# Kernel optimization log

Hardware: AMD Instinct MI355X
Metric: run time of the kernel (lower is better)

Reference implementation:

```python
import jax, jax.numpy as jnp
import numpy as np
from jax import lax

B, IN, H1, H2, NC = 16384, 128, 256, 128, 10
BETA = 0.5
THR = 1.0
SLOPE = 25.0  # snntorch surrogate.fast_sigmoid default slope


@jax.custom_vjp
def spike(x):
    # Heaviside fire with fast-sigmoid surrogate gradient
    return (x > 0).astype(x.dtype)

def _spike_fwd(x):
    return spike(x), x

def _spike_bwd(x, g):
    return (g / (SLOPE * jnp.abs(x) + 1.0) ** 2,)

spike.defvjp(_spike_fwd, _spike_bwd)


def setup_inputs() -> dict:
    key = jax.random.key(0)
    ks = jax.random.split(key, 7)
    def lin(kw, kb, fan_in, fan_out):
        lim = 1.0 / np.sqrt(fan_in)
        W = jax.random.uniform(kw, (fan_out, fan_in), jnp.float32, -lim, lim)
        b = jax.random.uniform(kb, (fan_out,), jnp.float32, -lim, lim)
        return W, b
    W1, b1 = lin(ks[0], ks[1], IN, H1)
    W2, b2 = lin(ks[2], ks[3], H1, H2)
    Wo, bo = lin(ks[4], ks[5], H2, NC)
    x = jax.random.normal(ks[6], (B, IN), jnp.float32)
    return {"x": x, "W1": W1, "b1": b1, "W2": W2, "b2": b2,
            "Wo": Wo, "bo": bo, "num_steps": 20}


def reference(x, W1, b1, W2, b2, Wo, bo, num_steps):
    # fc1(x) is time-invariant -> hoist out of the recurrent loop (same math)
    cur1 = x @ W1.T + b1  # [B, H1]

    def lif(mem, cur):
        # snntorch Leaky (reset_mechanism='subtract'):
        # reset from previous mem (detached), then decay+input, then fire
        reset = lax.stop_gradient((mem > THR).astype(mem.dtype))
        mem = BETA * mem + cur - reset * THR
        spk = spike(mem - THR)
        return spk, mem

    def step(carry, _):
        m1, m2, mo = carry
        s1, m1 = lif(m1, cur1)
        s2, m2 = lif(m2, s1 @ W2.T + b2)
        so, mo = lif(mo, s2 @ Wo.T + bo)
        return (m1, m2, mo), so

    init = (jnp.zeros((B, H1), x.dtype),
            jnp.zeros((B, H2), x.dtype),
            jnp.zeros((B, NC), x.dtype))
    _, spk_rec = lax.scan(step, init, None, length=num_steps)
    return spk_rec.sum(axis=0)  # [B, NC] spike counts
```

## Files before the change

kernel.cpp:

```cpp
#include <hip/hip_runtime.h>
#include <stdint.h>

#define B_TOT 16384
#define IN_DIM 128
#define H1 256
#define H2 128
#define NC 10

#define W2T_BYTES (H1 * H2 * 4)
#define WOT_OFF   W2T_BYTES
#define WOT_BYTES (H2 * NC * 4)
#define SCR_OFF   (WOT_OFF + WOT_BYTES)
#define LDS_BYTES (SCR_OFF + 16 * 1024)

typedef float v2f __attribute__((ext_vector_type(2)));

__global__ __launch_bounds__(256) void gemm1_kernel(
    const float* __restrict__ x, const float* __restrict__ W1,
    const float* __restrict__ b1, float* __restrict__ cur1) {
  __shared__ float xs[16 * 128];
  const int tid = threadIdx.x;
  const long row0 = (long)blockIdx.x * 16;

  const float4* xt = (const float4*)(x + row0 * IN_DIM);
  float4* xs4 = (float4*)xs;
  xs4[tid] = xt[tid];
  xs4[tid + 256] = xt[tid + 256];
  __syncthreads();

  const int n = tid;
  float acc[16];
#pragma unroll
  for (int r = 0; r < 16; ++r) acc[r] = 0.f;

  const float* wrow = W1 + n * IN_DIM;
  for (int k0 = 0; k0 < IN_DIM; k0 += 4) {
    const float4 wv = *(const float4*)(wrow + k0);
#pragma unroll
    for (int r = 0; r < 16; ++r) {
      const float4 xv = *(const float4*)(xs + r * IN_DIM + k0);
      acc[r] = fmaf(wv.x, xv.x, acc[r]);
      acc[r] = fmaf(wv.y, xv.y, acc[r]);
      acc[r] = fmaf(wv.z, xv.z, acc[r]);
      acc[r] = fmaf(wv.w, xv.w, acc[r]);
    }
  }
  const float bias = b1[n];
#pragma unroll
  for (int r = 0; r < 16; ++r)
    cur1[(row0 + r) * H1 + n] = acc[r] + bias;
}

__global__ __launch_bounds__(1024) void transpose_kernel(
    const float* __restrict__ W2, const float* __restrict__ Wo,
    float* __restrict__ W2T, float* __restrict__ WoT) {
  const int idx = blockIdx.x * 1024 + threadIdx.x;
  if (idx < H2 * H1) {
    const int o = idx >> 8;
    const int j = idx & 255;
    W2T[j * H2 + o] = W2[idx];
  } else {
    const int k = idx - H2 * H1;
    if (k < NC * H2) {
      const int o = k >> 7;
      const int j = k & 127;
      WoT[j * NC + o] = Wo[k];
    }
  }
}

__device__ __forceinline__ int mbcnt64(unsigned long long m) {
  return (int)__builtin_amdgcn_mbcnt_hi(
      (unsigned)(m >> 32), __builtin_amdgcn_mbcnt_lo((unsigned)m, 0u));
}

__device__ __noinline__ v2f serial_row(unsigned long long m0,
                                       unsigned long long m1,
                                       unsigned long long m2,
                                       unsigned long long m3,
                                       const char* w2b) {
  v2f acc = {0.f, 0.f};
  while (m0) { const int j = (int)__builtin_ctzll(m0); m0 &= m0 - 1;
    acc += *(const v2f*)(w2b + (j << 9)); }
  while (m1) { const int j = (int)__builtin_ctzll(m1); m1 &= m1 - 1;
    acc += *(const v2f*)(w2b + ((64 + j) << 9)); }
  while (m2) { const int j = (int)__builtin_ctzll(m2); m2 &= m2 - 1;
    acc += *(const v2f*)(w2b + ((128 + j) << 9)); }
  while (m3) { const int j = (int)__builtin_ctzll(m3); m3 &= m3 - 1;
    acc += *(const v2f*)(w2b + ((192 + j) << 9)); }
  return acc;
}

__global__ __launch_bounds__(1024) void snn_kernel(
    const float* __restrict__ cur1, const float* __restrict__ W2Tg,
    const float* __restrict__ WoTg, const float* __restrict__ b2,
    const float* __restrict__ bo, const int* __restrict__ nsp,
    float* __restrict__ out) {
  extern __shared__ float lds[];

  const int tid = threadIdx.x;
  {
    float4* dst = (float4*)lds;
    const float4* src = (const float4*)W2Tg;
#pragma unroll
    for (int i = 0; i < 8; ++i) dst[tid + i * 1024] = src[tid + i * 1024];
    if (tid < 320)
      ((float4*)((char*)lds + WOT_OFF))[tid] = ((const float4*)WoTg)[tid];
  }
  __syncthreads();

  const int w = tid >> 6;
  const int l = tid & 63;
  const int lo = (l < NC) ? l : 0;
  const float bb0 = b2[2 * l];
  const float bb1 = b2[2 * l + 1];
  const float bol = bo[lo];
  const int nsteps = *nsp;

  int* scrA = (int*)((char*)lds + SCR_OFF) + w * 256;
  int* scrB = scrA + 128;
  const char* w2b = (const char*)lds + 8 * l;
  const char* wob = (const char*)lds + WOT_OFF + 4 * lo;

  const int wr0 = l << 9;
  const int wr1 = (64 + l) << 9;
  const int wr2 = (128 + l) << 9;
  const int wr3 = (192 + l) << 9;
  const int or0 = 80 * l;
  const int or1 = 80 * l + 40;

#define LOAD8(P, scrp, kk)                                  \
  const int4 P##ia = *(const int4*)((scrp) + (kk));         \
  const int4 P##ib = *(const int4*)((scrp) + (kk) + 4);     \
  const v2f P##p0 = *(const v2f*)(w2b + P##ia.x);           \
  const v2f P##p1 = *(const v2f*)(w2b + P##ia.y);           \
  const v2f P##p2 = *(const v2f*)(w2b + P##ia.z);           \
  const v2f P##p3 = *(const v2f*)(w2b + P##ia.w);           \
  const v2f P##p4 = *(const v2f*)(w2b + P##ib.x);           \
  const v2f P##p5 = *(const v2f*)(w2b + P##ib.y);           \
  const v2f P##p6 = *(const v2f*)(w2b + P##ib.z);           \
  const v2f P##p7 = *(const v2f*)(w2b + P##ib.w);

#define ADD8(P, acc)                                        \
  acc += P##p0; acc += P##p1; acc += P##p2; acc += P##p3;   \
  acc += P##p4; acc += P##p5; acc += P##p6; acc += P##p7;

#define TAILS(scrp, S, acc)                                 \
  {                                                         \
    int k = ((S) >> 3) << 3;                                \
    if ((S) & 4) {                                          \
      const int4 ia = *(const int4*)((scrp) + k);           \
      const v2f p0 = *(const v2f*)(w2b + ia.x);             \
      const v2f p1 = *(const v2f*)(w2b + ia.y);             \
      const v2f p2 = *(const v2f*)(w2b + ia.z);             \
      const v2f p3 = *(const v2f*)(w2b + ia.w);             \
      acc += p0; acc += p1; acc += p2; acc += p3;           \
      k += 4;                                               \
    }                                                       \
    if ((S) & 2) {                                          \
      const int2 ia = *(const int2*)((scrp) + k);           \
      const v2f p0 = *(const v2f*)(w2b + ia.x);             \
      const v2f p1 = *(const v2f*)(w2b + ia.y);             \
      acc += p0; acc += p1;                                 \
      k += 2;                                               \
    }                                                       \
    if ((S) & 1) {                                          \
      const v2f p0 = *(const v2f*)(w2b + (scrp)[k]);        \
      acc += p0;                                            \
    }                                                       \
  }

#define OLOAD8(P, scrp, kk)                                 \
  const int4 P##ia = *(const int4*)((scrp) + (kk));         \
  const int4 P##ib = *(const int4*)((scrp) + (kk) + 4);     \
  const float P##q0 = *(const float*)(wob + P##ia.x);       \
  const float P##q1 = *(const float*)(wob + P##ia.y);       \
  const float P##q2 = *(const float*)(wob + P##ia.z);       \
  const float P##q3 = *(const float*)(wob + P##ia.w);       \
  const float P##q4 = *(const float*)(wob + P##ib.x);       \
  const float P##q5 = *(const float*)(wob + P##ib.y);       \
  const float P##q6 = *(const float*)(wob + P##ib.z);       \
  const float P##q7 = *(const float*)(wob + P##ib.w);

#define OADD8(P, co)                                        \
  co += P##q0; co += P##q1; co += P##q2; co += P##q3;       \
  co += P##q4; co += P##q5; co += P##q6; co += P##q7;

#define OTAILS(scrp, S, co)                                 \
  {                                                         \
    int k = ((S) >> 3) << 3;                                \
    if ((S) & 4) {                                          \
      const int4 ia = *(const int4*)((scrp) + k);           \
      const float u0 = *(const float*)(wob + ia.x);         \
      const float u1 = *(const float*)(wob + ia.y);         \
      const float u2 = *(const float*)(wob + ia.z);         \
      const float u3 = *(const float*)(wob + ia.w);         \
      co += u0; co += u1; co += u2; co += u3;               \
      k += 4;                                               \
    }                                                       \
    if ((S) & 2) {                                          \
      const int2 ia = *(const int2*)((scrp) + k);           \
      const float u0 = *(const float*)(wob + ia.x);         \
      const float u1 = *(const float*)(wob + ia.y);         \
      co += u0; co += u1;                                   \
      k += 2;                                               \
    }                                                       \
    if ((S) & 1) {                                          \
      co += *(const float*)(wob + (scrp)[k]);               \
    }                                                       \
  }

  for (int rp = 0; rp < 2; ++rp) {
    const long bA = (long)blockIdx.x * 64 + w * 4 + rp * 2;
    const long bB = bA + 1;

    float cA[4], cB[4];
#pragma unroll
    for (int i = 0; i < 4; ++i) {
      cA[i] = cur1[bA * H1 + i * 64 + l];
      cB[i] = cur1[bB * H1 + i * 64 + l];
    }

    float mA1[4] = {0.f, 0.f, 0.f, 0.f}, spA1[4] = {0.f, 0.f, 0.f, 0.f};
    float mB1[4] = {0.f, 0.f, 0.f, 0.f}, spB1[4] = {0.f, 0.f, 0.f, 0.f};
    float mA2a = 0.f, mA2b = 0.f, spA2a = 0.f, spA2b = 0.f;
    float mB2a = 0.f, mB2b = 0.f, spB2a = 0.f, spB2b = 0.f;
    float moA = 0.f, spoA = 0.f, cntA = 0.f;
    float moB = 0.f, spoB = 0.f, cntB = 0.f;

    for (int t = 0; t < nsteps; ++t) {
      unsigned long long gA[4], gB[4];
      bool sA[4], sB[4];
#pragma unroll
      for (int i = 0; i < 4; ++i) {
        mA1[i] = fmaf(0.5f, mA1[i], cA[i]) - spA1[i];
        sA[i] = mA1[i] > 1.0f;
        spA1[i] = sA[i] ? 1.0f : 0.0f;
        gA[i] = __ballot(sA[i]);
        mB1[i] = fmaf(0.5f, mB1[i], cB[i]) - spB1[i];
        sB[i] = mB1[i] > 1.0f;
        spB1[i] = sB[i] ? 1.0f : 0.0f;
        gB[i] = __ballot(sB[i]);
      }
      const int pA0 = (int)__popcll(gA[0]);
      const int pA01 = pA0 + (int)__popcll(gA[1]);
      const int pA012 = pA01 + (int)__popcll(gA[2]);
      const int SA = pA012 + (int)__popcll(gA[3]);
      const int pB0 = (int)__popcll(gB[0]);
      const int pB01 = pB0 + (int)__popcll(gB[1]);
      const int pB012 = pB01 + (int)__popcll(gB[2]);
      const int SB = pB012 + (int)__popcll(gB[3]);

      if (sA[0]) scrA[mbcnt64(gA[0])] = wr0;
      if (sA[1]) scrA[pA0 + mbcnt64(gA[1])] = wr1;
      if (sA[2]) { const int rk = pA01 + mbcnt64(gA[2]);
                   if (rk < 128) scrA[rk] = wr2; }
      if (sA[3]) { const int rk = pA012 + mbcnt64(gA[3]);
                   if (rk < 128) scrA[rk] = wr3; }
      if (sB[0]) scrB[mbcnt64(gB[0])] = wr0;
      if (sB[1]) scrB[pB0 + mbcnt64(gB[1])] = wr1;
      if (sB[2]) { const int rk = pB01 + mbcnt64(gB[2]);
                   if (rk < 128) scrB[rk] = wr2; }
      if (sB[3]) { const int rk = pB012 + mbcnt64(gB[3]);
                   if (rk < 128) scrB[rk] = wr3; }
      asm volatile("s_waitcnt lgkmcnt(0)" ::: "memory");

      v2f accA = {0.f, 0.f}, accB = {0.f, 0.f};
      if (__builtin_expect(SA > 128 || SB > 128, 0)) {
        accA = serial_row(gA[0], gA[1], gA[2], gA[3], w2b);
        accB = serial_row(gB[0], gB[1], gB[2], gB[3], w2b);
      } else {
        const int nA8 = SA >> 3;
        const int nB8 = SB >> 3;
        int ka = 0, kb = 0;
        while (ka < nA8 && kb < nB8) {
          { LOAD8(a_, scrA, ka * 8) LOAD8(b_, scrB, kb * 8)
            ADD8(a_, accA) ADD8(b_, accB) }
          ++ka; ++kb;
        }
        while (ka < nA8) {
          { LOAD8(c_, scrA, ka * 8) ADD8(c_, accA) }
          ++ka;
        }
        while (kb < nB8) {
          { LOAD8(d_, scrB, kb * 8) ADD8(d_, accB) }
          ++kb;
        }
        TAILS(scrA, SA, accA)
        TAILS(scrB, SB, accB)
      }
      const float aA0 = accA.x + bb0;
      const float aA1 = accA.y + bb1;
      const float aB0 = accB.x + bb0;
      const float aB1 = accB.y + bb1;

      mA2a = fmaf(0.5f, mA2a, aA0) - spA2a;
      mA2b = fmaf(0.5f, mA2b, aA1) - spA2b;
      mB2a = fmaf(0.5f, mB2a, aB0) - spB2a;
      mB2b = fmaf(0.5f, mB2b, aB1) - spB2b;
      const bool saA = mA2a > 1.0f, sbA = mA2b > 1.0f;
      const bool saB = mB2a > 1.0f, sbB = mB2b > 1.0f;
      const unsigned long long mAe = __ballot(saA);
      const unsigned long long mAo = __ballot(sbA);
      const unsigned long long mBe = __ballot(saB);
      const unsigned long long mBo = __ballot(sbB);
      spA2a = saA ? 1.0f : 0.0f;
      spA2b = sbA ? 1.0f : 0.0f;
      spB2a = saB ? 1.0f : 0.0f;
      spB2b = sbB ? 1.0f : 0.0f;
      const int pAe = (int)__popcll(mAe);
      const int SoA = pAe + (int)__popcll(mAo);
      const int pBe = (int)__popcll(mBe);
      const int SoB = pBe + (int)__popcll(mBo);

      if (saA) scrA[mbcnt64(mAe)] = or0;
      if (sbA) scrA[pAe + mbcnt64(mAo)] = or1;
      if (saB) scrB[mbcnt64(mBe)] = or0;
      if (sbB) scrB[pBe + mbcnt64(mBo)] = or1;
      asm volatile("s_waitcnt lgkmcnt(0)" ::: "memory");

      float coA = 0.f, coB = 0.f;
      {
        const int nA8 = SoA >> 3;
        const int nB8 = SoB >> 3;
        int ka = 0, kb = 0;
        while (ka < nA8 && kb < nB8) {
          { OLOAD8(e_, scrA, ka * 8) OLOAD8(f_, scrB, kb * 8)
            OADD8(e_, coA) OADD8(f_, coB) }
          ++ka; ++kb;
        }
        while (ka < nA8) {
          { OLOAD8(g_, scrA, ka * 8) OADD8(g_, coA) }
          ++ka;
        }
        while (kb < nB8) {
          { OLOAD8(h_, scrB, kb * 8) OADD8(h_, coB) }
          ++kb;
        }
        OTAILS(scrA, SoA, coA)
        OTAILS(scrB, SoB, coB)
      }
      coA += bol;
      coB += bol;

      moA = fmaf(0.5f, moA, coA) - spoA;
      moB = fmaf(0.5f, moB, coB) - spoB;
      const bool soA = moA > 1.0f;
      const bool soB = moB > 1.0f;
      spoA = soA ? 1.0f : 0.0f;
      spoB = soB ? 1.0f : 0.0f;
      cntA += spoA;
      cntB += spoB;
    }

    if (l < NC) {
      out[bA * NC + l] = cntA;
      out[bB * NC + l] = cntB;
    }
  }
#undef LOAD8
#undef ADD8
#undef TAILS
#undef OLOAD8
#undef OADD8
#undef OTAILS
}

extern "C" void kernel_launch(void* const* d_in, const int* in_sizes, int n_in,
                              void* d_out, int out_size, void* d_ws,
                              size_t ws_size, hipStream_t stream) {
  const float* x  = (const float*)d_in[0];
  const float* W1 = (const float*)d_in[1];
  const float* b1 = (const float*)d_in[2];
  const float* W2 = (const float*)d_in[3];
  const float* b2 = (const float*)d_in[4];
  const float* Wo = (const float*)d_in[5];
  const float* bo = (const float*)d_in[6];
  const int* nsp  = (const int*)d_in[7];
  float* outp = (float*)d_out;

  float* cur1 = (float*)d_ws;
  float* W2Tg = cur1 + (size_t)B_TOT * H1;
  float* WoTg = W2Tg + H1 * H2;

  gemm1_kernel<<<B_TOT / 16, 256, 0, stream>>>(x, W1, b1, cur1);
  transpose_kernel<<<(H2 * H1 + NC * H2 + 1023) / 1024, 1024, 0, stream>>>(
      W2, Wo, W2Tg, WoTg);

  hipFuncSetAttribute((const void*)snn_kernel,
                      hipFuncAttributeMaxDynamicSharedMemorySize, LDS_BYTES);
  snn_kernel<<<256, 1024, LDS_BYTES, stream>>>(cur1, W2Tg, WoTg, b2, bo, nsp,
                                               outp);
}
```

Before: 115.4 us.

## Fuse transpose into gemm1, register-tile gemm1, interleave four rows per wave

Folds the weight transpose into an extra block of the first GEMM launch, which removes one kernel launch. The GEMM now uses 64-row blocks with a 4x16 register tile per thread, so each x load from LDS feeds more FMAs. The SNN kernel processes four batch rows per wave at once instead of two pairs in sequence, giving more independent LDS gathers to overlap latency. The scratch list per row shrinks to 64 entries, with a serial fallback when more than 64 spikes fire; this costs more registers and the fallback path is taken more often.

Measured after the change: 157.0 us. +36.0%, slower.

```diff
diff --git a/kernel.cpp b/kernel.cpp
--- a/kernel.cpp
+++ b/kernel.cpp
@@ -15,57 +15,81 @@
 
 typedef float v2f __attribute__((ext_vector_type(2)));
 
-__global__ __launch_bounds__(256) void gemm1_kernel(
+__global__ __launch_bounds__(256) void gemm1_fused_kernel(
     const float* __restrict__ x, const float* __restrict__ W1,
-    const float* __restrict__ b1, float* __restrict__ cur1) {
-  __shared__ float xs[16 * 128];
+    const float* __restrict__ b1, const float* __restrict__ W2,
+    const float* __restrict__ Wo, float* __restrict__ cur1,
+    float* __restrict__ W2T, float* __restrict__ WoT) {
   const int tid = threadIdx.x;
-  const long row0 = (long)blockIdx.x * 16;
-
+  if (blockIdx.x == 256) {
+    for (int idx = tid; idx < H2 * H1; idx += 256) {
+      const int o = idx >> 8;
+      const int j = idx & 255;
+      W2T[j * H2 + o] = W2[idx];
+    }
+    for (int idx = tid; idx < NC * H2; idx += 256) {
+      const int o = idx >> 7;
+      const int j = idx & 127;
+      WoT[j * NC + o] = Wo[idx];
+    }
+    return;
+  }
+
+  __shared__ float xs[64 * 128];
+  const long row0 = (long)blockIdx.x * 64;
   const float4* xt = (const float4*)(x + row0 * IN_DIM);
   float4* xs4 = (float4*)xs;
-  xs4[tid] = xt[tid];
-  xs4[tid + 256] = xt[tid + 256];
+#pragma unroll
+  for (int i = 0; i < 8; ++i) xs4[tid + i * 256] = xt[tid + i * 256];
   __syncthreads();
 
-  const int n = tid;
-  float acc[16];
-#pragma unroll
-  for (int r = 0; r < 16; ++r) acc[r] = 0.f;
-
-  const float* wrow = W1 + n * IN_DIM;
+  const int n0 = 4 * (tid & 63);
+  const int rb = 16 * (tid >> 6);
+
+  float4 acc[16];
+#pragma unroll
+  for (int r = 0; r < 16; ++r) acc[r] = make_float4(0.f, 0.f, 0.f, 0.f);
+
+  const float* w0p = W1 + (n0 + 0) * IN_DIM;
+  const float* w1p = W1 + (n0 + 1) * IN_DIM;
+  const float* w2p = W1 + (n0 + 2) * IN_DIM;
+  const float* w3p = W1 + (n0 + 3) * IN_DIM;
+
   for (int k0 = 0; k0 < IN_DIM; k0 += 4) {
-    const float4 wv = *(const float4*)(wrow + k0);
+    const float4 w0 = *(const float4*)(w0p + k0);
+    const float4 w1 = *(const float4*)(w1p + k0);
+    const float4 w2 = *(const float4*)(w2p + k0);
+    const float4 w3 = *(const float4*)(w3p + k0);
 #pragma unroll
     for (int r = 0; r < 16; ++r) {
-      const float4 xv = *(const float4*)(xs + r * IN_DIM + k0);
-      acc[r] = fmaf(wv.x, xv.x, acc[r]);
-      acc[r] = fmaf(wv.y, xv.y, acc[r]);
-      acc[r] = fmaf(wv.z, xv.z, acc[r]);
-      acc[r] = fmaf(wv.w, xv.w, acc[r]);
-    }
-  }
-  const float bias = b1[n];
-#pragma unroll
-  for (int r = 0; r < 16; ++r)
-    cur1[(row0 + r) * H1 + n] = acc[r] + bias;
-}
-
-__global__ __launch_bounds__(1024) void transpose_kernel(
-    const float* __restrict__ W2, const float* __restrict__ Wo,
-    float* __restrict__ W2T, float* __restrict__ WoT) {
-  const int idx = blockIdx.x * 1024 + threadIdx.x;
-  if (idx < H2 * H1) {
-    const int o = idx >> 8;
-    const int j = idx & 255;
-    W2T[j * H2 + o] = W2[idx];
-  } else {
-    const int k = idx - H2 * H1;
-    if (k < NC * H2) {
-      const int o = k >> 7;
-      const int j = k & 127;
-      WoT[j * NC + o] = Wo[k];
-    }
+      const float4 xv = *(const float4*)(xs + (rb + r) * IN_DIM + k0);
+      acc[r].x = fmaf(w0.x, xv.x, acc[r].x);
+      acc[r].x = fmaf(w0.y, xv.y, acc[r].x);
+      acc[r].x = fmaf(w0.z, xv.z, acc[r].x);
+      acc[r].x = fmaf(w0.w, xv.w, acc[r].x);
+      acc[r].y = fmaf(w1.x, xv.x, acc[r].y);
+      acc[r].y = fmaf(w1.y, xv.y, acc[r].y);
+      acc[r].y = fmaf(w1.z, xv.z, acc[r].y);
+      acc[r].y = fmaf(w1.w, xv.w, acc[r].y);
+      acc[r].z = fmaf(w2.x, xv.x, acc[r].z);
+      acc[r].z = fmaf(w2.y, xv.y, acc[r].z);
+      acc[r].z = fmaf(w2.z, xv.z, acc[r].z);
+      acc[r].z = fmaf(w2.w, xv.w, acc[r].z);
+      acc[r].w = fmaf(w3.x, xv.x, acc[r].w);
+      acc[r].w = fmaf(w3.y, xv.y, acc[r].w);
+      acc[r].w = fmaf(w3.z, xv.z, acc[r].w);
+      acc[r].w = fmaf(w3.w, xv.w, acc[r].w);
+    }
+  }
+  const float4 bias = *(const float4*)(b1 + n0);
+#pragma unroll
+  for (int r = 0; r < 16; ++r) {
+    float4 o;
+    o.x = acc[r].x + bias.x;
+    o.y = acc[r].y + bias.y;
+    o.z = acc[r].z + bias.z;
+    o.w = acc[r].w + bias.w;
+    *(float4*)(cur1 + (row0 + rb + r) * H1 + n0) = o;
   }
 }
 
@@ -74,11 +98,12 @@
       (unsigned)(m >> 32), __builtin_amdgcn_mbcnt_lo((unsigned)m, 0u));
 }
 
-__device__ __noinline__ v2f serial_row(unsigned long long m0,
-                                       unsigned long long m1,
-                                       unsigned long long m2,
-                                       unsigned long long m3,
-                                       const char* w2b) {
+__device__ __noinline__ v2f serial_main(float n0, float n1, float n2, float n3,
+                                        const char* w2b) {
+  unsigned long long m0 = __ballot(n0 > 1.0f);
+  unsigned long long m1 = __ballot(n1 > 1.0f);
+  unsigned long long m2 = __ballot(n2 > 1.0f);
+  unsigned long long m3 = __ballot(n3 > 1.0f);
   v2f acc = {0.f, 0.f};
   while (m0) { const int j = (int)__builtin_ctzll(m0); m0 &= m0 - 1;
     acc += *(const v2f*)(w2b + (j << 9)); }
@@ -91,6 +116,18 @@
   return acc;
 }
 
+__device__ __noinline__ float serial_out(float m2a, float m2b,
+                                         const char* wob) {
+  unsigned long long me = __ballot(m2a > 1.0f);
+  unsigned long long mo = __ballot(m2b > 1.0f);
+  float co = 0.f;
+  while (me) { const int j = (int)__builtin_ctzll(me); me &= me - 1;
+    co += *(const float*)(wob + j * 80); }
+  while (mo) { const int j = (int)__builtin_ctzll(mo); mo &= mo - 1;
+    co += *(const float*)(wob + j * 80 + 40); }
+  return co;
+}
+
 __global__ __launch_bounds__(1024) void snn_kernel(
     const float* __restrict__ cur1, const float* __restrict__ W2Tg,
     const float* __restrict__ WoTg, const float* __restrict__ b2,
@@ -117,8 +154,11 @@
   const float bol = bo[lo];
   const int nsteps = *nsp;
 
-  int* scrA = (int*)((char*)lds + SCR_OFF) + w * 256;
-  int* scrB = scrA + 128;
+  int* scr = (int*)((char*)lds + SCR_OFF) + w * 256;
+  int* sA = scr;
+  int* sB = scr + 64;
+  int* sC = scr + 128;
+  int* sD = scr + 192;
   const char* w2b = (const char*)lds + 8 * l;
   const char* wob = (const char*)lds + WOT_OFF + 4 * lo;
 
@@ -210,153 +250,195 @@
     }                                                       \
   }
 
-  for (int rp = 0; rp < 2; ++rp) {
-    const long bA = (long)blockIdx.x * 64 + w * 4 + rp * 2;
-    const long bB = bA + 1;
-
-    float cA[4], cB[4];
-#pragma unroll
-    for (int i = 0; i < 4; ++i) {
-      cA[i] = cur1[bA * H1 + i * 64 + l];
-      cB[i] = cur1[bB * H1 + i * 64 + l];
-    }
-
-    float mA1[4] = {0.f, 0.f, 0.f, 0.f}, spA1[4] = {0.f, 0.f, 0.f, 0.f};
-    float mB1[4] = {0.f, 0.f, 0.f, 0.f}, spB1[4] = {0.f, 0.f, 0.f, 0.f};
-    float mA2a = 0.f, mA2b = 0.f, spA2a = 0.f, spA2b = 0.f;
-    float mB2a = 0.f, mB2b = 0.f, spB2a = 0.f, spB2b = 0.f;
-    float moA = 0.f, spoA = 0.f, cntA = 0.f;
-    float moB = 0.f, spoB = 0.f, cntB = 0.f;
-
-    for (int t = 0; t < nsteps; ++t) {
-      unsigned long long gA[4], gB[4];
-      bool sA[4], sB[4];
+#define BUILD_MAIN(sq, s0, s1, s2, s3, g0, g1, g2, g3, p0, p01, p012)  \
+  if (s0) (sq)[mbcnt64(g0)] = wr0;                                     \
+  if (s1) { const int rk = (p0) + mbcnt64(g1);                         \
+            if (rk < 64) (sq)[rk] = wr1; }                             \
+  if (s2) { const int rk = (p01) + mbcnt64(g2);                        \
+            if (rk < 64) (sq)[rk] = wr2; }                             \
+  if (s3) { const int rk = (p012) + mbcnt64(g3);                       \
+            if (rk < 64) (sq)[rk] = wr3; }
+
+  const long b0 = (long)blockIdx.x * 64 + w * 4;
+
+  float c[4][4];
+#pragma unroll
+  for (int q = 0; q < 4; ++q)
+#pragma unroll
+    for (int i = 0; i < 4; ++i) c[q][i] = cur1[(b0 + q) * H1 + i * 64 + l];
+
+  float m1v[4][4], sp1[4][4];
+#pragma unroll
+  for (int q = 0; q < 4; ++q)
+#pragma unroll
+    for (int i = 0; i < 4; ++i) { m1v[q][i] = 0.f; sp1[q][i] = 0.f; }
+  float m2a[4] = {0.f, 0.f, 0.f, 0.f}, m2b[4] = {0.f, 0.f, 0.f, 0.f};
+  float sp2a[4] = {0.f, 0.f, 0.f, 0.f}, sp2b[4] = {0.f, 0.f, 0.f, 0.f};
+  float mo[4] = {0.f, 0.f, 0.f, 0.f}, spo[4] = {0.f, 0.f, 0.f, 0.f};
+  float cnt[4] = {0.f, 0.f, 0.f, 0.f};
+
+  for (int t = 0; t < nsteps; ++t) {
+    unsigned long long g[4][4];
+    bool s[4][4];
+    int S[4], pA[4], pAB[4], pABC[4];
+#pragma unroll
+    for (int q = 0; q < 4; ++q) {
 #pragma unroll
       for (int i = 0; i < 4; ++i) {
-        mA1[i] = fmaf(0.5f, mA1[i], cA[i]) - spA1[i];
-        sA[i] = mA1[i] > 1.0f;
-        spA1[i] = sA[i] ? 1.0f : 0.0f;
-        gA[i] = __ballot(sA[i]);
-        mB1[i] = fmaf(0.5f, mB1[i], cB[i]) - spB1[i];
-        sB[i] = mB1[i] > 1.0f;
-        spB1[i] = sB[i] ? 1.0f : 0.0f;
-        gB[i] = __ballot(sB[i]);
-      }
-      const int pA0 = (int)__popcll(gA[0]);
-      const int pA01 = pA0 + (int)__popcll(gA[1]);
-      const int pA012 = pA01 + (int)__popcll(gA[2]);
-      const int SA = pA012 + (int)__popcll(gA[3]);
-      const int pB0 = (int)__popcll(gB[0]);
-      const int pB01 = pB0 + (int)__popcll(gB[1]);
-      const int pB012 = pB01 + (int)__popcll(gB[2]);
-      const int SB = pB012 + (int)__popcll(gB[3]);
-
-      if (sA[0]) scrA[mbcnt64(gA[0])] = wr0;
-      if (sA[1]) scrA[pA0 + mbcnt64(gA[1])] = wr1;
-      if (sA[2]) { const int rk = pA01 + mbcnt64(gA[2]);
-                   if (rk < 128) scrA[rk] = wr2; }
-      if (sA[3]) { const int rk = pA012 + mbcnt64(gA[3]);
-                   if (rk < 128) scrA[rk] = wr3; }
-      if (sB[0]) scrB[mbcnt64(gB[0])] = wr0;
-      if (sB[1]) scrB[pB0 + mbcnt64(gB[1])] = wr1;
-      if (sB[2]) { const int rk = pB01 + mbcnt64(gB[2]);
-                   if (rk < 128) scrB[rk] = wr2; }
-      if (sB[3]) { const int rk = pB012 + mbcnt64(gB[3]);
-                   if (rk < 128) scrB[rk] = wr3; }
-      asm volatile("s_waitcnt lgkmcnt(0)" ::: "memory");
-
-      v2f accA = {0.f, 0.f}, accB = {0.f, 0.f};
-      if (__builtin_expect(SA > 128 || SB > 128, 0)) {
-        accA = serial_row(gA[0], gA[1], gA[2], gA[3], w2b);
-        accB = serial_row(gB[0], gB[1], gB[2], gB[3], w2b);
-      } else {
-        const int nA8 = SA >> 3;
-        const int nB8 = SB >> 3;
-        int ka = 0, kb = 0;
-        while (ka < nA8 && kb < nB8) {
-          { LOAD8(a_, scrA, ka * 8) LOAD8(b_, scrB, kb * 8)
-            ADD8(a_, accA) ADD8(b_, accB) }
-          ++ka; ++kb;
-        }
-        while (ka < nA8) {
-          { LOAD8(c_, scrA, ka * 8) ADD8(c_, accA) }
-          ++ka;
-        }
-        while (kb < nB8) {
-          { LOAD8(d_, scrB, kb * 8) ADD8(d_, accB) }
-          ++kb;
-        }
-        TAILS(scrA, SA, accA)
-        TAILS(scrB, SB, accB)
-      }
-      const float aA0 = accA.x + bb0;
-      const float aA1 = accA.y + bb1;
-      const float aB0 = accB.x + bb0;
-      const float aB1 = accB.y + bb1;
-
-      mA2a = fmaf(0.5f, mA2a, aA0) - spA2a;
-      mA2b = fmaf(0.5f, mA2b, aA1) - spA2b;
-      mB2a = fmaf(0.5f, mB2a, aB0) - spB2a;
-      mB2b = fmaf(0.5f, mB2b, aB1) - spB2b;
-      const bool saA = mA2a > 1.0f, sbA = mA2b > 1.0f;
-      const bool saB = mB2a > 1.0f, sbB = mB2b > 1.0f;
-      const unsigned long long mAe = __ballot(saA);
-      const unsigned long long mAo = __ballot(sbA);
-      const unsigned long long mBe = __ballot(saB);
-      const unsigned long long mBo = __ballot(sbB);
-      spA2a = saA ? 1.0f : 0.0f;
-      spA2b = sbA ? 1.0f : 0.0f;
-      spB2a = saB ? 1.0f : 0.0f;
-      spB2b = sbB ? 1.0f : 0.0f;
-      const int pAe = (int)__popcll(mAe);
-      const int SoA = pAe + (int)__popcll(mAo);
-      const int pBe = (int)__popcll(mBe);
-      const int SoB = pBe + (int)__popcll(mBo);
-
-      if (saA) scrA[mbcnt64(mAe)] = or0;
-      if (sbA) scrA[pAe + mbcnt64(mAo)] = or1;
-      if (saB) scrB[mbcnt64(mBe)] = or0;
-      if (sbB) scrB[pBe + mbcnt64(mBo)] = or1;
-      asm volatile("s_waitcnt lgkmcnt(0)" ::: "memory");
-
-      float coA = 0.f, coB = 0.f;
-      {
-        const int nA8 = SoA >> 3;
-        const int nB8 = SoB >> 3;
-        int ka = 0, kb = 0;
-        while (ka < nA8 && kb < nB8) {
-          { OLOAD8(e_, scrA, ka * 8) OLOAD8(f_, scrB, kb * 8)
-            OADD8(e_, coA) OADD8(f_, coB) }
-          ++ka; ++kb;
-        }
-        while (ka < nA8) {
-          { OLOAD8(g_, scrA, ka * 8) OADD8(g_, coA) }
-          ++ka;
-        }
-        while (kb < nB8) {
-          { OLOAD8(h_, scrB, kb * 8) OADD8(h_, coB) }
-          ++kb;
-        }
-        OTAILS(scrA, SoA, coA)
-        OTAILS(scrB, SoB, coB)
-      }
-      coA += bol;
-      coB += bol;
-
-      moA = fmaf(0.5f, moA, coA) - spoA;
-      moB = fmaf(0.5f, moB, coB) - spoB;
-      const bool soA = moA > 1.0f;
-      const bool soB = moB > 1.0f;
-      spoA = soA ? 1.0f : 0.0f;
-      spoB = soB ? 1.0f : 0.0f;
-      cntA += spoA;
-      cntB += spoB;
-    }
-
-    if (l < NC) {
-      out[bA * NC + l] = cntA;
-      out[bB * NC + l] = cntB;
-    }
+        m1v[q][i] = fmaf(0.5f, m1v[q][i], c[q][i]) - sp1[q][i];
+        s[q][i] = m1v[q][i] > 1.0f;
+        sp1[q][i] = s[q][i] ? 1.0f : 0.0f;
+        g[q][i] = __ballot(s[q][i]);
+      }
+      pA[q] = (int)__popcll(g[q][0]);
+      pAB[q] = pA[q] + (int)__popcll(g[q][1]);
+      pABC[q] = pAB[q] + (int)__popcll(g[q][2]);
+      S[q] = pABC[q] + (int)__popcll(g[q][3]);
+    }
+
+    BUILD_MAIN(sA, s[0][0], s[0][1], s[0][2], s[0][3],
+               g[0][0], g[0][1], g[0][2], g[0][3], pA[0], pAB[0], pABC[0])
+    BUILD_MAIN(sB, s[1][0], s[1][1], s[1][2], s[1][3],
+               g[1][0], g[1][1], g[1][2], g[1][3], pA[1], pAB[1], pABC[1])
+    BUILD_MAIN(sC, s[2][0], s[2][1], s[2][2], s[2][3],
+               g[2][0], g[2][1], g[2][2], g[2][3], pA[2], pAB[2], pABC[2])
+    BUILD_MAIN(sD, s[3][0], s[3][1], s[3][2], s[3][3],
+               g[3][0], g[3][1], g[3][2], g[3][3], pA[3], pAB[3], pABC[3])
+    asm volatile("s_waitcnt lgkmcnt(0)" ::: "memory");
+
+    v2f acc0 = {0.f, 0.f}, acc1 = {0.f, 0.f};
+    v2f acc2 = {0.f, 0.f}, acc3 = {0.f, 0.f};
+    if (__builtin_expect(S[0] > 64 || S[1] > 64 || S[2] > 64 || S[3] > 64,
+                         0)) {
+      acc0 = serial_main(m1v[0][0], m1v[0][1], m1v[0][2], m1v[0][3], w2b);
+      acc1 = serial_main(m1v[1][0], m1v[1][1], m1v[1][2], m1v[1][3], w2b);
+      acc2 = serial_main(m1v[2][0], m1v[2][1], m1v[2][2], m1v[2][3], w2b);
+      acc3 = serial_main(m1v[3][0], m1v[3][1], m1v[3][2], m1v[3][3], w2b);
+    } else {
+      const int na = S[0] >> 3, nb = S[1] >> 3;
+      const int nc_ = S[2] >> 3, nd = S[3] >> 3;
+      int ka = 0, kb = 0, kc = 0, kd = 0;
+      while (ka < na && kb < nb && kc < nc_ && kd < nd) {
+        { LOAD8(a_, sA, ka * 8) LOAD8(b_, sB, kb * 8)
+          LOAD8(c_, sC, kc * 8) LOAD8(d_, sD, kd * 8)
+          ADD8(a_, acc0) ADD8(b_, acc1) ADD8(c_, acc2) ADD8(d_, acc3) }
+        ++ka; ++kb; ++kc; ++kd;
+      }
+      while (ka < na && kb < nb) {
+        { LOAD8(e_, sA, ka * 8) LOAD8(f_, sB, kb * 8)
+          ADD8(e_, acc0) ADD8(f_, acc1) }
+        ++ka; ++kb;
+      }
+      while (kc < nc_ && kd < nd) {
+        { LOAD8(i_, sC, kc * 8) LOAD8(j_, sD, kd * 8)
+          ADD8(i_, acc2) ADD8(j_, acc3) }
+        ++kc; ++kd;
+      }
+      while (ka < na) { { LOAD8(k_, sA, ka * 8) ADD8(k_, acc0) } ++ka; }
+      while (kb < nb) { { LOAD8(l_, sB, kb * 8) ADD8(l_, acc1) } ++kb; }
+      while (kc < nc_) { { LOAD8(m_, sC, kc * 8) ADD8(m_, acc2) } ++kc; }
+      while (kd < nd) { { LOAD8(n_, sD, kd * 8) ADD8(n_, acc3) } ++kd; }
+      TAILS(sA, S[0], acc0)
+      TAILS(sB, S[1], acc1)
+      TAILS(sC, S[2], acc2)
+      TAILS(sD, S[3], acc3)
+    }
+
+    const float a00 = acc0.x + bb0, a01 = acc0.y + bb1;
+    const float a10 = acc1.x + bb0, a11 = acc1.y + bb1;
+    const float a20 = acc2.x + bb0, a21 = acc2.y + bb1;
+    const float a30 = acc3.x + bb0, a31 = acc3.y + bb1;
+    m2a[0] = fmaf(0.5f, m2a[0], a00) - sp2a[0];
+    m2b[0] = fmaf(0.5f, m2b[0], a01) - sp2b[0];
+    m2a[1] = fmaf(0.5f, m2a[1], a10) - sp2a[1];
+    m2b[1] = fmaf(0.5f, m2b[1], a11) - sp2b[1];
+    m2a[2] = fmaf(0.5f, m2a[2], a20) - sp2a[2];
+    m2b[2] = fmaf(0.5f, m2b[2], a21) - sp2b[2];
+    m2a[3] = fmaf(0.5f, m2a[3], a30) - sp2a[3];
+    m2b[3] = fmaf(0.5f, m2b[3], a31) - sp2b[3];
+
+    unsigned long long me[4], mod[4];
+    int So[4], pe[4];
+#pragma unroll
+    for (int q = 0; q < 4; ++q) {
+      const bool sa = m2a[q] > 1.0f;
+      const bool sb = m2b[q] > 1.0f;
+      me[q] = __ballot(sa);
+      mod[q] = __ballot(sb);
+      sp2a[q] = sa ? 1.0f : 0.0f;
+      sp2b[q] = sb ? 1.0f : 0.0f;
+      pe[q] = (int)__popcll(me[q]);
+      So[q] = pe[q] + (int)__popcll(mod[q]);
+    }
+
+#pragma unroll
+    for (int q = 0; q < 4; ++q) {
+      int* sq = scr + q * 64;
+      if (sp2a[q] != 0.f) sq[mbcnt64(me[q])] = or0;
+      if (sp2b[q] != 0.f) {
+        const int rk = pe[q] + mbcnt64(mod[q]);
+        if (rk < 64) sq[rk] = or1;
+      }
+    }
+    asm volatile("s_waitcnt lgkmcnt(0)" ::: "memory");
+
+    float co0 = 0.f, co1 = 0.f, co2 = 0.f, co3 = 0.f;
+    if (__builtin_expect(So[0] > 64 || So[1] > 64 || So[2] > 64 ||
+                             So[3] > 64,
+                         0)) {
+      co0 = serial_out(m2a[0], m2b[0], wob);
+      co1 = serial_out(m2a[1], m2b[1], wob);
+      co2 = serial_out(m2a[2], m2b[2], wob);
+      co3 = serial_out(m2a[3], m2b[3], wob);
+    } else {
+      const int na = So[0] >> 3, nb = So[1] >> 3;
+      const int nc_ = So[2] >> 3, nd = So[3] >> 3;
+      int ka = 0, kb = 0, kc = 0, kd = 0;
+      while (ka < na && kb < nb && kc < nc_ && kd < nd) {
+        { OLOAD8(a_, sA, ka * 8) OLOAD8(b_, sB, kb * 8)
+          OLOAD8(c_, sC, kc * 8) OLOAD8(d_, sD, kd * 8)
+          OADD8(a_, co0) OADD8(b_, co1) OADD8(c_, co2) OADD8(d_, co3) }
+        ++ka; ++kb; ++kc; ++kd;
+      }
+      while (ka < na && kb < nb) {
+        { OLOAD8(e_, sA, ka * 8) OLOAD8(f_, sB, kb * 8)
+          OADD8(e_, co0) OADD8(f_, co1) }
+        ++ka; ++kb;
+      }
+      while (kc < nc_ && kd < nd) {
+        { OLOAD8(i_, sC, kc * 8) OLOAD8(j_, sD, kd * 8)
+          OADD8(i_, co2) OADD8(j_, co3) }
+        ++kc; ++kd;
+      }
+      while (ka < na) { { OLOAD8(k_, sA, ka * 8) OADD8(k_, co0) } ++ka; }
+      while (kb < nb) { { OLOAD8(l_, sB, kb * 8) OADD8(l_, co1) } ++kb; }
+      while (kc < nc_) { { OLOAD8(m_, sC, kc * 8) OADD8(m_, co2) } ++kc; }
+      while (kd < nd) { { OLOAD8(n_, sD, kd * 8) OADD8(n_, co3) } ++kd; }
+      OTAILS(sA, So[0], co0)
+      OTAILS(sB, So[1], co1)
+      OTAILS(sC, So[2], co2)
+      OTAILS(sD, So[3], co3)
+    }
+    co0 += bol;
+    co1 += bol;
+    co2 += bol;
+    co3 += bol;
+
+    mo[0] = fmaf(0.5f, mo[0], co0) - spo[0];
+    mo[1] = fmaf(0.5f, mo[1], co1) - spo[1];
+    mo[2] = fmaf(0.5f, mo[2], co2) - spo[2];
+    mo[3] = fmaf(0.5f, mo[3], co3) - spo[3];
+#pragma unroll
+    for (int q = 0; q < 4; ++q) {
+      const bool so = mo[q] > 1.0f;
+      spo[q] = so ? 1.0f : 0.0f;
+      cnt[q] += spo[q];
+    }
+  }
+
+  if (l < NC) {
+#pragma unroll
+    for (int q = 0; q < 4; ++q) out[(b0 + q) * NC + l] = cnt[q];
   }
 #undef LOAD8
 #undef ADD8
@@ -364,6 +446,7 @@
 #undef OLOAD8
 #undef OADD8
 #undef OTAILS
+#undef BUILD_MAIN
 }
 
 extern "C" void kernel_launch(void* const* d_in, const int* in_sizes, int n_in,
@@ -383,9 +466,8 @@
   float* W2Tg = cur1 + (size_t)B_TOT * H1;
   float* WoTg = W2Tg + H1 * H2;
 
-  gemm1_kernel<<<B_TOT / 16, 256, 0, stream>>>(x, W1, b1, cur1);
-  transpose_kernel<<<(H2 * H1 + NC * H2 + 1023) / 1024, 1024, 0, stream>>>(
-      W2, Wo, W2Tg, WoTg);
+  gemm1_fused_kernel<<<257, 256, 0, stream>>>(x, W1, b1, W2, Wo, cur1, W2Tg,
+                                              WoTg);
 
   hipFuncSetAttribute((const void*)snn_kernel,
                       hipFuncAttributeMaxDynamicSharedMemorySize, LDS_BYTES);
```

## Fuse first-layer GEMM into SNN kernel, dropping cur1 workspace round trip

Applied to the files above, without the earlier changes.

Removes the separate gemm1 kernel and computes each lane's fc1 outputs for its two batch rows directly inside the SNN kernel, reading x and W1 from global memory. This avoids writing and re-reading the 16 MB cur1 intermediate and one kernel launch. In exchange, the fc1 compute is no longer tiled through shared memory: each lane streams a W1 row from global/L2, and x loads are broadcast across the wave. That may be less efficient per FLOP and lengthens the serial prologue of the 1024-thread blocks.

Result: slower. 227.4 us (+97.0%).

```diff
diff --git a/kernel.cpp b/kernel.cpp
--- a/kernel.cpp
+++ b/kernel.cpp
@@ -14,42 +14,6 @@
 #define LDS_BYTES (SCR_OFF + 16 * 1024)
 
 typedef float v2f __attribute__((ext_vector_type(2)));
-
-__global__ __launch_bounds__(256) void gemm1_kernel(
-    const float* __restrict__ x, const float* __restrict__ W1,
-    const float* __restrict__ b1, float* __restrict__ cur1) {
-  __shared__ float xs[16 * 128];
-  const int tid = threadIdx.x;
-  const long row0 = (long)blockIdx.x * 16;
-
-  const float4* xt = (const float4*)(x + row0 * IN_DIM);
-  float4* xs4 = (float4*)xs;
-  xs4[tid] = xt[tid];
-  xs4[tid + 256] = xt[tid + 256];
-  __syncthreads();
-
-  const int n = tid;
-  float acc[16];
-#pragma unroll
-  for (int r = 0; r < 16; ++r) acc[r] = 0.f;
-
-  const float* wrow = W1 + n * IN_DIM;
-  for (int k0 = 0; k0 < IN_DIM; k0 += 4) {
-    const float4 wv = *(const float4*)(wrow + k0);
-#pragma unroll
-    for (int r = 0; r < 16; ++r) {
-      const float4 xv = *(const float4*)(xs + r * IN_DIM + k0);
-      acc[r] = fmaf(wv.x, xv.x, acc[r]);
-      acc[r] = fmaf(wv.y, xv.y, acc[r]);
-      acc[r] = fmaf(wv.z, xv.z, acc[r]);
-      acc[r] = fmaf(wv.w, xv.w, acc[r]);
-    }
-  }
-  const float bias = b1[n];
-#pragma unroll
-  for (int r = 0; r < 16; ++r)
-    cur1[(row0 + r) * H1 + n] = acc[r] + bias;
-}
 
 __global__ __launch_bounds__(1024) void transpose_kernel(
     const float* __restrict__ W2, const float* __restrict__ Wo,
@@ -92,7 +56,8 @@
 }
 
 __global__ __launch_bounds__(1024) void snn_kernel(
-    const float* __restrict__ cur1, const float* __restrict__ W2Tg,
+    const float* __restrict__ x, const float* __restrict__ W1,
+    const float* __restrict__ b1, const float* __restrict__ W2Tg,
     const float* __restrict__ WoTg, const float* __restrict__ b2,
     const float* __restrict__ bo, const int* __restrict__ nsp,
     float* __restrict__ out) {
@@ -215,10 +180,31 @@
     const long bB = bA + 1;
 
     float cA[4], cB[4];
+    {
+      const float* xrA = x + bA * IN_DIM;
+      const float* xrB = x + bB * IN_DIM;
 #pragma unroll
-    for (int i = 0; i < 4; ++i) {
-      cA[i] = cur1[bA * H1 + i * 64 + l];
-      cB[i] = cur1[bB * H1 + i * 64 + l];
+      for (int i = 0; i < 4; ++i) {
+        const int n = i * 64 + l;
+        const float* wr = W1 + n * IN_DIM;
+        float aA = 0.f, aB = 0.f;
+        for (int k0 = 0; k0 < IN_DIM; k0 += 4) {
+          const float4 wv = *(const float4*)(wr + k0);
+          const float4 xA = *(const float4*)(xrA + k0);
+          const float4 xB = *(const float4*)(xrB + k0);
+          aA = fmaf(wv.x, xA.x, aA);
+          aA = fmaf(wv.y, xA.y, aA);
+          aA = fmaf(wv.z, xA.z, aA);
+          aA = fmaf(wv.w, xA.w, aA);
+          aB = fmaf(wv.x, xB.x, aB);
+          aB = fmaf(wv.y, xB.y, aB);
+          aB = fmaf(wv.z, xB.z, aB);
+          aB = fmaf(wv.w, xB.w, aB);
+        }
+        const float bias = b1[n];
+        cA[i] = aA + bias;
+        cB[i] = aB + bias;
+      }
     }
 
     float mA1[4] = {0.f, 0.f, 0.f, 0.f}, spA1[4] = {0.f, 0.f, 0.f, 0.f};
@@ -379,16 +365,14 @@
   const int* nsp  = (const int*)d_in[7];
   float* outp = (float*)d_out;
 
-  float* cur1 = (float*)d_ws;
-  float* W2Tg = cur1 + (size_t)B_TOT * H1;
+  float* W2Tg = (float*)d_ws;
   float* WoTg = W2Tg + H1 * H2;
 
-  gemm1_kernel<<<B_TOT / 16, 256, 0, stream>>>(x, W1, b1, cur1);
   transpose_kernel<<<(H2 * H1 + NC * H2 + 1023) / 1024, 1024, 0, stream>>>(
       W2, Wo, W2Tg, WoTg);
 
   hipFuncSetAttribute((const void*)snn_kernel,
                       hipFuncAttributeMaxDynamicSharedMemorySize, LDS_BYTES);
-  snn_kernel<<<256, 1024, LDS_BYTES, stream>>>(cur1, W2Tg, WoTg, b2, bo, nsp,
-                                               outp);
-}
+  snn_kernel<<<256, 1024, LDS_BYTES, stream>>>(x, W1, b1, W2Tg, WoTg, b2, bo,
+                                               nsp, outp);
+}
```
